# Kernel tuning notes

Measured on AMD Instinct MI355X. Metric: run time of the kernel, lower is better.

Reference implementation:

```python
import jax, jax.numpy as jnp
import numpy as np

H = 128  # hidden size

def _lstm_layer(x, Wih, Whh, bih, bhh):
    # x: [B, T, D]; Wih: [4H, D]; Whh: [4H, H]; biases: [4H]
    B, T, _ = x.shape
    # Precompute input contribution for all timesteps (one big GEMM)
    xg = jnp.einsum('btd,gd->btg', x, Wih) + bih + bhh  # [B, T, 4H]
    xg = jnp.swapaxes(xg, 0, 1)  # time-major [T, B, 4H]

    def step(carry, xt):
        h, c = carry
        gates = xt + h @ Whh.T  # [B, 4H]
        i, f, g, o = jnp.split(gates, 4, axis=-1)
        i = jax.nn.sigmoid(i)
        f = jax.nn.sigmoid(f)
        g = jnp.tanh(g)
        o = jax.nn.sigmoid(o)
        c = f * c + i * g
        h = o * jnp.tanh(c)
        return (h, c), h

    h0 = jnp.zeros((B, H), dtype=x.dtype)
    c0 = jnp.zeros((B, H), dtype=x.dtype)
    (_, _), hs = jax.lax.scan(step, (h0, c0), xg)
    return jnp.swapaxes(hs, 0, 1)  # [B, T, H]


def setup_inputs() -> dict:
    key = jax.random.key(0)
    ks = jax.random.split(key, 9)
    B, T, D = 32, 2048, 64
    s0 = 1.0 / np.sqrt(H)
    x = jax.random.normal(ks[0], (B, T, D), dtype=jnp.float32)
    # layer 0: input dim 64, layer 1: input dim 128 (torch gate order i,f,g,o)
    Wih0 = jax.random.uniform(ks[1], (4 * H, D), jnp.float32, -s0, s0)
    Whh0 = jax.random.uniform(ks[2], (4 * H, H), jnp.float32, -s0, s0)
    bih0 = jax.random.uniform(ks[3], (4 * H,), jnp.float32, -s0, s0)
    bhh0 = jax.random.uniform(ks[4], (4 * H,), jnp.float32, -s0, s0)
    Wih1 = jax.random.uniform(ks[5], (4 * H, H), jnp.float32, -s0, s0)
    Whh1 = jax.random.uniform(ks[6], (4 * H, H), jnp.float32, -s0, s0)
    bih1 = jax.random.uniform(ks[7], (4 * H,), jnp.float32, -s0, s0)
    bhh1 = jax.random.uniform(ks[8], (4 * H,), jnp.float32, -s0, s0)
    return {"x": x, "Wih0": Wih0, "Whh0": Whh0, "bih0": bih0, "bhh0": bhh0,
            "Wih1": Wih1, "Whh1": Whh1, "bih1": bih1, "bhh1": bhh1}


def reference(x, Wih0, Whh0, bih0, bhh0, Wih1, Whh1, bih1, bhh1):
    h = _lstm_layer(x, Wih0, Whh0, bih0, bhh0)
    h = _lstm_layer(h, Wih1, Whh1, bih1, bhh1)
    return h  # [B, T, H] full hidden-state sequence of the top layer
```

## Files before the change

kernel.cpp:

```cpp
#include <hip/hip_runtime.h>

#define TLEN 2048
#define BATCH 32
#define DIN 64
#define HID 128
#define RING 256
#define CHK 8
#define WRS 68

typedef _Float16 f16;
typedef _Float16 h2 __attribute__((ext_vector_type(2)));
typedef float f4 __attribute__((ext_vector_type(4)));
typedef unsigned int u32;

#if defined(__has_builtin)
#if __has_builtin(__builtin_amdgcn_fdot2)
#define FDOT2(a, b, c) __builtin_amdgcn_fdot2((a), (b), (c), false)
#endif
#endif
#ifndef FDOT2
#define FDOT2(a, b, c) ((c) + (float)(a).x * (float)(b).x + (float)(a).y * (float)(b).y)
#endif
#define DOT2U(wu, hv, acc) FDOT2(__builtin_bit_cast(h2, (wu)), (hv), (acc))

#if defined(__has_builtin)
#if __has_builtin(__builtin_amdgcn_exp2f)
#define FEXP2(x) __builtin_amdgcn_exp2f(x)
#endif
#if __has_builtin(__builtin_amdgcn_rcpf)
#define FRCP(x) __builtin_amdgcn_rcpf(x)
#endif
#endif
#ifndef FEXP2
#define FEXP2(x) __expf((x) * 0.69314718f)
#endif
#ifndef FRCP
#define FRCP(x) (1.0f / (x))
#endif

__device__ __forceinline__ float sigm(float x) {
    return FRCP(1.0f + FEXP2(-1.44269504f * x));
}
__device__ __forceinline__ float tanh_c(float x) {
    x = fminf(fmaxf(x, -15.0f), 15.0f);
    float e = FEXP2(2.88539008f * x);
    return (e - 1.0f) * FRCP(e + 1.0f);
}
__device__ __forceinline__ void qreduce(float (&v)[4]) {
    #pragma unroll
    for (int m = 0; m < 4; ++m) {
        v[m] += __shfl_xor(v[m], 1, 4);
        v[m] += __shfl_xor(v[m], 2, 4);
    }
}

__device__ __forceinline__ u32 aload_rlx(const u32* p) {
    return __hip_atomic_load(p, __ATOMIC_RELAXED, __HIP_MEMORY_SCOPE_AGENT);
}
__device__ __forceinline__ u32 aload_acq(const u32* p) {
    return __hip_atomic_load(p, __ATOMIC_ACQUIRE, __HIP_MEMORY_SCOPE_AGENT);
}
__device__ __forceinline__ void astore_rlx(u32* p, u32 v) {
    __hip_atomic_store(p, v, __ATOMIC_RELAXED, __HIP_MEMORY_SCOPE_AGENT);
}
__device__ __forceinline__ void astore_rel(u32* p, u32 v) {
    __hip_atomic_store(p, v, __ATOMIC_RELEASE, __HIP_MEMORY_SCOPE_AGENT);
}

__device__ __forceinline__ void stage_weights(const float* __restrict__ W,
                                              u32* __restrict__ wl, int t0) {
    const float2* src2 = (const float2*)W;
    for (int idx = t0; idx < 512 * 64; idx += 512) {
        const int row = idx >> 6, d = idx & 63;
        float2 v = src2[(size_t)row * 64 + d];
        h2 x; x.x = (f16)v.x; x.y = (f16)v.y;
        wl[(size_t)row * WRS + d] = __builtin_bit_cast(u32, x);
    }
}

__device__ __forceinline__ void dot_wlds(const u32* __restrict__ wl,
                                         int rg, int kg,
                                         const u32* __restrict__ hsl,
                                         float (&p)[4]) {
    uint4 hq[4];
    #pragma unroll
    for (int i4 = 0; i4 < 4; ++i4) hq[i4] = *(const uint4*)&hsl[i4 * 4];
    #pragma unroll
    for (int m = 0; m < 4; ++m) {
        const u32* wb = wl + (size_t)(rg + 128 * m) * WRS + kg * 16;
        #pragma unroll
        for (int i4 = 0; i4 < 4; ++i4) {
            const uint4 wq = *(const uint4*)&wb[i4 * 4];
            const u32* hw = (const u32*)&hq[i4];
            p[m] = DOT2U(wq.x, __builtin_bit_cast(h2, hw[0]), p[m]);
            p[m] = DOT2U(wq.y, __builtin_bit_cast(h2, hw[1]), p[m]);
            p[m] = DOT2U(wq.z, __builtin_bit_cast(h2, hw[2]), p[m]);
            p[m] = DOT2U(wq.w, __builtin_bit_cast(h2, hw[3]), p[m]);
        }
    }
}

__global__ __launch_bounds__(512) void xg_precompute(
    const float* __restrict__ X, const float* __restrict__ Wih0,
    const float* __restrict__ bih0, const float* __restrict__ bhh0,
    f16* __restrict__ XG)
{
    __shared__ float xs[16][DIN];
    const int blk = blockIdx.x;
    const int b   = blk / (TLEN / 16);
    const int tc  = blk % (TLEN / 16);
    const int j   = threadIdx.x;
    const int row = (j >> 2) + 128 * (j & 3);

    const float* xsrc = X + ((size_t)b * TLEN + (size_t)tc * 16) * DIN;
    for (int i = j; i < 16 * DIN; i += 512) ((float*)xs)[i] = xsrc[i];
    __syncthreads();

    f4 w[16];
    const f4* wp = (const f4*)(Wih0 + (size_t)row * DIN);
    #pragma unroll
    for (int i = 0; i < 16; ++i) w[i] = wp[i];
    const float bias = bih0[row] + bhh0[row];

    f16* dst = XG + ((size_t)b * TLEN + (size_t)tc * 16) * 512 + j;
    #pragma unroll 4
    for (int t = 0; t < 16; ++t) {
        float acc = bias;
        const f4* xv = (const f4*)&xs[t][0];
        #pragma unroll
        for (int i = 0; i < 16; ++i) {
            f4 x4 = xv[i];
            acc += w[i][0] * x4[0] + w[i][1] * x4[1] + w[i][2] * x4[2] + w[i][3] * x4[3];
        }
        dst[(size_t)t * 512] = (f16)acc;
    }
}

__global__ __launch_bounds__(512) void lstm2_pipe(
    const f16* __restrict__ XG0,
    const float* __restrict__ Whh0,
    const float* __restrict__ Wih1, const float* __restrict__ Whh1,
    const float* __restrict__ bih1, const float* __restrict__ bhh1,
    float* __restrict__ Out,
    u32* __restrict__ H0g,
    u32* __restrict__ XG1,
    u32* __restrict__ Flags)
{
    __shared__ alignas(16) u32 pool[39040];

    const int role = blockIdx.x / BATCH;
    const int b    = blockIdx.x % BATCH;
    const int t0   = threadIdx.x;
    const int rg   = t0 >> 2;
    const int kg   = t0 & 3;

    u32* F0 = Flags + (size_t)b * 16;
    u32* F1 = Flags + (size_t)(32 + b) * 16;
    u32* C2 = Flags + (size_t)(64 + b) * 16;

    if (role == 0) {
        stage_weights(Whh0, pool, t0);
        u32* hl = pool + 34816;
        if (t0 < 128) hl[t0] = 0u;
        float c0 = 0.0f;
        const f16* xgp = XG0 + (size_t)b * TLEN * 512 + t0;
        u32* h0out = H0g + (size_t)b * TLEN * 64;
        f16 xga = xgp[0];
        f16 xgb = xgp[512];
        __syncthreads();

        for (int t = 0; t < TLEN; ++t) {
            const int cur = t & 1, prv = cur ^ 1;
            const float xgv = (float)xga;
            xga = xgb;
            { int tn = (t + 2 < TLEN) ? t + 2 : TLEN - 1; xgb = xgp[(size_t)tn * 512]; }

            float p[4];
            #pragma unroll
            for (int m = 0; m < 4; ++m) p[m] = (kg == m) ? xgv : 0.0f;
            dot_wlds(pool, rg, kg, hl + prv * 64 + kg * 16, p);
            qreduce(p);
            float ii = sigm(p[0]), ff = sigm(p[1]);
            float gg = tanh_c(p[2]), oo = sigm(p[3]);
            c0 = ff * c0 + ii * gg;
            if (kg == 0) {
                h2 hv2; hv2.x = (f16)(oo * tanh_c(c0)); hv2.y = hv2.x;
                f16* hf = (f16*)(hl + cur * 64);
                hf[rg] = hv2.x;
            }
            __syncthreads();
            if (t0 < 64)
                astore_rlx(&h0out[(size_t)t * 64 + t0], hl[cur * 64 + t0]);
            if (t0 == 0 && (t & (CHK - 1)) == (CHK - 1))
                astore_rel(F0, (u32)(t + 1));
        }
    } else if (role == 1) {
        stage_weights(Wih1, pool, t0);
        u32* h0c = pool + 34816;
        const int rowk = rg + 128 * kg;
        const float B1 = bih1[rowk] + bhh1[rowk];
        u32* H0in = H0g + (size_t)b * TLEN * 64;
        u32* xout = XG1 + (size_t)b * RING * 512;
        u32 sc = 0;
        __syncthreads();

        for (int c = 0; c < TLEN / CHK; ++c) {
            const int tbase = c * CHK;
            if (t0 == 0) {
                u32 av; long g = 0;
                do { av = aload_acq(F0);
                     if (av >= (u32)(tbase + CHK)) break;
                     __builtin_amdgcn_s_sleep(2);
                } while (++g < 50000000L);
                if (tbase + CHK > (int)sc + (RING - 64)) {
                    g = 0;
                    do { sc = aload_rlx(C2);
                         if (tbase + CHK <= (int)sc + (RING - 64)) break;
                         __builtin_amdgcn_s_sleep(2);
                    } while (++g < 50000000L);
                }
            }
            __syncthreads();
            h0c[t0] = aload_rlx(&H0in[(size_t)tbase * 64 + t0]);
            __syncthreads();

            #pragma unroll
            for (int s = 0; s < CHK; ++s) {
                const int t = tbase + s;
                float p[4];
                #pragma unroll
                for (int m = 0; m < 4; ++m) p[m] = (kg == m) ? B1 : 0.0f;
                dot_wlds(pool, rg, kg, h0c + s * 64 + kg * 16, p);
                qreduce(p);
                astore_rlx(&xout[(size_t)(t & (RING - 1)) * 512 + t0],
                           __builtin_bit_cast(u32, p[kg]));
            }
            asm volatile("s_waitcnt vmcnt(0)" ::: "memory");
            __syncthreads();
            if (t0 == 0) astore_rel(F1, (u32)(tbase + CHK));
        }
    } else {
        stage_weights(Whh1, pool, t0);
        u32* xgc = pool + 34816;
        u32* hl  = pool + 38912;
        if (t0 < 128) hl[t0] = 0u;
        u32* xin = XG1 + (size_t)b * RING * 512;
        float c1 = 0.0f;
        __syncthreads();

        for (int c = 0; c < TLEN / CHK; ++c) {
            const int tbase = c * CHK;
            if (t0 == 0) {
                u32 av; long g = 0;
                do { av = aload_acq(F1);
                     if (av >= (u32)(tbase + CHK)) break;
                     __builtin_amdgcn_s_sleep(2);
                } while (++g < 50000000L);
            }
            __syncthreads();
            const size_t rbase = (size_t)(tbase & (RING - 1)) * 512;
            #pragma unroll
            for (int k = 0; k < CHK; ++k)
                xgc[k * 512 + t0] = aload_rlx(&xin[rbase + k * 512 + t0]);
            __syncthreads();

            #pragma unroll 1
            for (int s = 0; s < CHK; ++s) {
                const int t = tbase + s;
                const int cur = t & 1, prv = cur ^ 1;
                const float xgv = __builtin_bit_cast(float, xgc[s * 512 + t0]);

                float q[4];
                #pragma unroll
                for (int m = 0; m < 4; ++m) q[m] = (kg == m) ? xgv : 0.0f;
                dot_wlds(pool, rg, kg, hl + prv * 64 + kg * 16, q);
                qreduce(q);
                float ii = sigm(q[0]), ff = sigm(q[1]);
                float gg = tanh_c(q[2]), oo = sigm(q[3]);
                c1 = ff * c1 + ii * gg;
                float h1v = oo * tanh_c(c1);
                if (kg == 0) {
                    f16* hf = (f16*)(hl + cur * 64);
                    hf[rg] = (f16)h1v;
                    Out[((size_t)b * TLEN + t) * HID + rg] = h1v;
                }
                __syncthreads();
            }
            if (t0 == 0 && (c & 3) == 3)
                astore_rlx(C2, (u32)(tbase + CHK));
        }
    }
}

__global__ __launch_bounds__(512, 2) void lstm2_persist(
    const float* __restrict__ X,
    const float* __restrict__ Wih0, const float* __restrict__ Whh0,
    const float* __restrict__ bih0, const float* __restrict__ bhh0,
    const float* __restrict__ Wih1, const float* __restrict__ Whh1,
    const float* __restrict__ bih1, const float* __restrict__ bhh1,
    float* __restrict__ Out)
{
    __shared__ unsigned int wih0_lds[512 * 33];
    __shared__ f16 h0buf[2][HID];
    __shared__ f16 h1buf[2][HID];

    const int b  = blockIdx.x;
    const int t  = threadIdx.x;
    const int rg = t >> 2;
    const int kg = t & 3;

    {
        const float2* src = (const float2*)(Wih0 + t * DIN);
        #pragma unroll
        for (int i = 0; i < 32; ++i) {
            float2 v = src[i];
            h2 p; p.x = (f16)v.x; p.y = (f16)v.y;
            wih0_lds[t * 33 + i] = __builtin_bit_cast(unsigned int, p);
        }
    }
    if (t < HID) {
        h0buf[0][t] = (f16)0.0f; h0buf[1][t] = (f16)0.0f;
        h1buf[0][t] = (f16)0.0f; h1buf[1][t] = (f16)0.0f;
    }

    h2 whh0[4][16], wih1[4][16], whh1[4][16];
    float bi0[4], bi1[4];
    #pragma unroll
    for (int m = 0; m < 4; ++m) {
        const int row = rg + 128 * m;
        const float2* a = (const float2*)(Whh0 + row * HID + kg * 32);
        const float2* c = (const float2*)(Wih1 + row * HID + kg * 32);
        const float2* d = (const float2*)(Whh1 + row * HID + kg * 32);
        #pragma unroll
        for (int i = 0; i < 16; ++i) {
            float2 v; h2 w;
            v = a[i]; w.x = (f16)v.x; w.y = (f16)v.y; whh0[m][i] = w;
            v = c[i]; w.x = (f16)v.x; w.y = (f16)v.y; wih1[m][i] = w;
            v = d[i]; w.x = (f16)v.x; w.y = (f16)v.y; whh1[m][i] = w;
        }
        bi0[m] = (kg == 0) ? (bih0[row] + bhh0[row]) : 0.0f;
        bi1[m] = (kg == 0) ? (bih1[row] + bhh1[row]) : 0.0f;
    }

    float c0 = 0.0f, c1 = 0.0f;
    __syncthreads();

    f4 xA[4], xB[4];
    {
        const f4* xp = (const f4*)(X + ((size_t)b * TLEN) * DIN + kg * 16);
        #pragma unroll
        for (int j = 0; j < 4; ++j) xA[j] = xp[j];
    }

    auto step = [&](int tt, f4 (&xc)[4], f4 (&xn)[4]) {
        const int cur = tt & 1, nxt = cur ^ 1;
        h2 xh[8];
        const float* xf = (const float*)xc;
        #pragma unroll
        for (int j = 0; j < 8; ++j) {
            h2 p; p.x = (f16)xf[2 * j]; p.y = (f16)xf[2 * j + 1];
            xh[j] = p;
        }
        {
            const int tn = (tt + 1 < TLEN) ? tt + 1 : TLEN - 1;
            const f4* xp = (const f4*)(X + ((size_t)b * TLEN + tn) * DIN + kg * 16);
            #pragma unroll
            for (int j = 0; j < 4; ++j) xn[j] = xp[j];
        }
        float p0[4];
        #pragma unroll
        for (int m = 0; m < 4; ++m) p0[m] = bi0[m];
        #pragma unroll
        for (int m = 0; m < 4; ++m) {
            const unsigned int* wr = &wih0_lds[(rg + 128 * m) * 33 + kg * 8];
            #pragma unroll
            for (int i = 0; i < 8; ++i) {
                h2 w = __builtin_bit_cast(h2, wr[i]);
                p0[m] = FDOT2(w, xh[i], p0[m]);
            }
        }
        {
            const unsigned int* hr = (const unsigned int*)&h0buf[cur][0];
            #pragma unroll
            for (int i = 0; i < 16; ++i) {
                h2 hv = __builtin_bit_cast(h2, hr[kg * 16 + i]);
                #pragma unroll
                for (int m = 0; m < 4; ++m)
                    p0[m] = FDOT2(whh0[m][i], hv, p0[m]);
            }
        }
        qreduce(p0);
        {
            float ii = sigm(p0[0]), ff = sigm(p0[1]);
            float gg = tanh_c(p0[2]), oo = sigm(p0[3]);
            c0 = ff * c0 + ii * gg;
            float h0v = oo * tanh_c(c0);
            if (kg == 0) h0buf[nxt][rg] = (f16)h0v;
        }
        __syncthreads();
        float q[4];
        #pragma unroll
        for (int m = 0; m < 4; ++m) q[m] = bi1[m];
        {
            const unsigned int* hr = (const unsigned int*)&h0buf[nxt][0];
            #pragma unroll
            for (int i = 0; i < 16; ++i) {
                h2 hv = __builtin_bit_cast(h2, hr[kg * 16 + i]);
                #pragma unroll
                for (int m = 0; m < 4; ++m)
                    q[m] = FDOT2(wih1[m][i], hv, q[m]);
            }
        }
        {
            const unsigned int* hr = (const unsigned int*)&h1buf[cur][0];
            #pragma unroll
            for (int i = 0; i < 16; ++i) {
                h2 hv = __builtin_bit_cast(h2, hr[kg * 16 + i]);
                #pragma unroll
                for (int m = 0; m < 4; ++m)
                    q[m] = FDOT2(whh1[m][i], hv, q[m]);
            }
        }
        qreduce(q);
        {
            float ii = sigm(q[0]), ff = sigm(q[1]);
            float gg = tanh_c(q[2]), oo = sigm(q[3]);
            c1 = ff * c1 + ii * gg;
            float h1v = oo * tanh_c(c1);
            if (kg == 0) {
                h1buf[nxt][rg] = (f16)h1v;
                Out[((size_t)b * TLEN + tt) * HID + rg] = h1v;
            }
        }
        __syncthreads();
    };

    for (int tt = 0; tt < TLEN; tt += 2) {
        step(tt, xA, xB);
        step(tt + 1, xB, xA);
    }
}

extern "C" void kernel_launch(void* const* d_in, const int* in_sizes, int n_in,
                              void* d_out, int out_size, void* d_ws, size_t ws_size,
                              hipStream_t stream) {
    const float* X    = (const float*)d_in[0];
    const float* Wih0 = (const float*)d_in[1];
    const float* Whh0 = (const float*)d_in[2];
    const float* bih0 = (const float*)d_in[3];
    const float* bhh0 = (const float*)d_in[4];
    const float* Wih1 = (const float*)d_in[5];
    const float* Whh1 = (const float*)d_in[6];
    const float* bih1 = (const float*)d_in[7];
    const float* bhh1 = (const float*)d_in[8];
    float* Out = (float*)d_out;

    const size_t XG0_B  = (size_t)BATCH * TLEN * 512 * 2;
    const size_t H0_B   = (size_t)BATCH * TLEN * 64 * 4;
    const size_t XG1_B  = (size_t)BATCH * RING * 512 * 4;
    const size_t FLAG_B = 96 * 16 * 4;
    const size_t NEED   = XG0_B + H0_B + XG1_B + FLAG_B;

    if (ws_size >= NEED) {
        char* ws = (char*)d_ws;
        f16* XG0   = (f16*)ws;
        u32* H0g   = (u32*)(ws + XG0_B);
        u32* XG1   = (u32*)(ws + XG0_B + H0_B);
        u32* Flags = (u32*)(ws + XG0_B + H0_B + XG1_B);

        hipMemsetAsync(Flags, 0, FLAG_B, stream);
        xg_precompute<<<dim3(BATCH * (TLEN / 16)), dim3(512), 0, stream>>>(
            X, Wih0, bih0, bhh0, XG0);
        lstm2_pipe<<<dim3(3 * BATCH), dim3(512), 0, stream>>>(
            XG0, Whh0, Wih1, Whh1, bih1, bhh1, Out, H0g, XG1, Flags);
    } else {
        lstm2_persist<<<dim3(BATCH), dim3(512), 0, stream>>>(
            X, Wih0, Whh0, bih0, bhh0, Wih1, Whh1, bih1, bhh1, Out);
    }
}
```

Before: 2.160 ms.

## Split recurrent weights between LDS and per-step global loads

Only the first two gate blocks (i,f) of each weight matrix are staged in LDS. The g,o halves are prepacked into a coalesced fp16 global layout by a new kernel and reloaded from global/L2 at every timestep, where an asm barrier stops them being hoisted into registers. LDS use per block drops from about 156KB to about 86KB, which cuts the LDS read traffic per step and may allow better occupancy or co-residency. The cost is 128 bytes per thread of global loads on the latency-critical recurrent path each step.

```diff
diff --git a/kernel.cpp b/kernel.cpp
--- a/kernel.cpp
+++ b/kernel.cpp
@@ -67,10 +67,10 @@
     __hip_atomic_store(p, v, __ATOMIC_RELEASE, __HIP_MEMORY_SCOPE_AGENT);
 }
 
-__device__ __forceinline__ void stage_weights(const float* __restrict__ W,
-                                              u32* __restrict__ wl, int t0) {
+__device__ __forceinline__ void stage_w2(const float* __restrict__ W,
+                                         u32* __restrict__ wl, int t0) {
     const float2* src2 = (const float2*)W;
-    for (int idx = t0; idx < 512 * 64; idx += 512) {
+    for (int idx = t0; idx < 256 * 64; idx += 512) {
         const int row = idx >> 6, d = idx & 63;
         float2 v = src2[(size_t)row * 64 + d];
         h2 x; x.x = (f16)v.x; x.y = (f16)v.y;
@@ -78,25 +78,64 @@
     }
 }
 
-__device__ __forceinline__ void dot_wlds(const u32* __restrict__ wl,
+__device__ __forceinline__ void dot_step(const u32* __restrict__ wl,
                                          int rg, int kg,
                                          const u32* __restrict__ hsl,
-                                         float (&p)[4]) {
+                                         uintptr_t wga, float (&p)[4]) {
+    uint4 wq[8];
+    const uint4* wgp = (const uint4*)wga;
+    #pragma unroll
+    for (int qq = 0; qq < 8; ++qq) wq[qq] = wgp[(size_t)qq * 512];
+
     uint4 hq[4];
     #pragma unroll
     for (int i4 = 0; i4 < 4; ++i4) hq[i4] = *(const uint4*)&hsl[i4 * 4];
-    #pragma unroll
-    for (int m = 0; m < 4; ++m) {
+
+    #pragma unroll
+    for (int m = 0; m < 2; ++m) {
         const u32* wb = wl + (size_t)(rg + 128 * m) * WRS + kg * 16;
         #pragma unroll
         for (int i4 = 0; i4 < 4; ++i4) {
-            const uint4 wq = *(const uint4*)&wb[i4 * 4];
+            const uint4 wv = *(const uint4*)&wb[i4 * 4];
             const u32* hw = (const u32*)&hq[i4];
-            p[m] = DOT2U(wq.x, __builtin_bit_cast(h2, hw[0]), p[m]);
-            p[m] = DOT2U(wq.y, __builtin_bit_cast(h2, hw[1]), p[m]);
-            p[m] = DOT2U(wq.z, __builtin_bit_cast(h2, hw[2]), p[m]);
-            p[m] = DOT2U(wq.w, __builtin_bit_cast(h2, hw[3]), p[m]);
-        }
+            p[m] = DOT2U(wv.x, __builtin_bit_cast(h2, hw[0]), p[m]);
+            p[m] = DOT2U(wv.y, __builtin_bit_cast(h2, hw[1]), p[m]);
+            p[m] = DOT2U(wv.z, __builtin_bit_cast(h2, hw[2]), p[m]);
+            p[m] = DOT2U(wv.w, __builtin_bit_cast(h2, hw[3]), p[m]);
+        }
+    }
+    #pragma unroll
+    for (int mh = 0; mh < 2; ++mh) {
+        #pragma unroll
+        for (int i4 = 0; i4 < 4; ++i4) {
+            const uint4 wv = wq[mh * 4 + i4];
+            const u32* hw = (const u32*)&hq[i4];
+            p[2 + mh] = DOT2U(wv.x, __builtin_bit_cast(h2, hw[0]), p[2 + mh]);
+            p[2 + mh] = DOT2U(wv.y, __builtin_bit_cast(h2, hw[1]), p[2 + mh]);
+            p[2 + mh] = DOT2U(wv.z, __builtin_bit_cast(h2, hw[2]), p[2 + mh]);
+            p[2 + mh] = DOT2U(wv.w, __builtin_bit_cast(h2, hw[3]), p[2 + mh]);
+        }
+    }
+}
+
+__global__ __launch_bounds__(512) void w_prepack(
+    const float* __restrict__ W0, const float* __restrict__ W1,
+    const float* __restrict__ W2, u32* __restrict__ WG)
+{
+    const float* W = (blockIdx.x == 0) ? W0 : (blockIdx.x == 1) ? W1 : W2;
+    u32* dst = WG + (size_t)blockIdx.x * 16384;
+    const int t0 = threadIdx.x, rg = t0 >> 2, kg = t0 & 3;
+    #pragma unroll
+    for (int qq = 0; qq < 8; ++qq) {
+        const int m = 2 + (qq >> 2), j = qq & 3;
+        const float* s = W + (size_t)(rg + 128 * m) * HID + kg * 32 + j * 8;
+        u32 out[4];
+        #pragma unroll
+        for (int d = 0; d < 4; ++d) {
+            h2 x; x.x = (f16)s[2 * d]; x.y = (f16)s[2 * d + 1];
+            out[d] = __builtin_bit_cast(u32, x);
+        }
+        *(uint4*)&dst[((size_t)qq * 512 + t0) * 4] = *(const uint4*)out;
     }
 }
 
@@ -144,9 +183,10 @@
     float* __restrict__ Out,
     u32* __restrict__ H0g,
     u32* __restrict__ XG1,
-    u32* __restrict__ Flags)
+    u32* __restrict__ Flags,
+    const u32* __restrict__ WG)
 {
-    __shared__ alignas(16) u32 pool[39040];
+    __shared__ alignas(16) u32 pool[21632];
 
     const int role = blockIdx.x / BATCH;
     const int b    = blockIdx.x % BATCH;
@@ -158,9 +198,11 @@
     u32* F1 = Flags + (size_t)(32 + b) * 16;
     u32* C2 = Flags + (size_t)(64 + b) * 16;
 
+    uintptr_t wga = (uintptr_t)(WG + (size_t)role * 16384 + (size_t)t0 * 4);
+
     if (role == 0) {
-        stage_weights(Whh0, pool, t0);
-        u32* hl = pool + 34816;
+        stage_w2(Whh0, pool, t0);
+        u32* hl = pool + 17408;
         if (t0 < 128) hl[t0] = 0u;
         float c0 = 0.0f;
         const f16* xgp = XG0 + (size_t)b * TLEN * 512 + t0;
@@ -175,18 +217,18 @@
             xga = xgb;
             { int tn = (t + 2 < TLEN) ? t + 2 : TLEN - 1; xgb = xgp[(size_t)tn * 512]; }
 
+            asm volatile("" : "+v"(wga));
             float p[4];
             #pragma unroll
             for (int m = 0; m < 4; ++m) p[m] = (kg == m) ? xgv : 0.0f;
-            dot_wlds(pool, rg, kg, hl + prv * 64 + kg * 16, p);
+            dot_step(pool, rg, kg, hl + prv * 64 + kg * 16, wga, p);
             qreduce(p);
             float ii = sigm(p[0]), ff = sigm(p[1]);
             float gg = tanh_c(p[2]), oo = sigm(p[3]);
             c0 = ff * c0 + ii * gg;
             if (kg == 0) {
-                h2 hv2; hv2.x = (f16)(oo * tanh_c(c0)); hv2.y = hv2.x;
                 f16* hf = (f16*)(hl + cur * 64);
-                hf[rg] = hv2.x;
+                hf[rg] = (f16)(oo * tanh_c(c0));
             }
             __syncthreads();
             if (t0 < 64)
@@ -195,8 +237,8 @@
                 astore_rel(F0, (u32)(t + 1));
         }
     } else if (role == 1) {
-        stage_weights(Wih1, pool, t0);
-        u32* h0c = pool + 34816;
+        stage_w2(Wih1, pool, t0);
+        u32* h0c = pool + 17408;
         const int rowk = rg + 128 * kg;
         const float B1 = bih1[rowk] + bhh1[rowk];
         u32* H0in = H0g + (size_t)b * TLEN * 64;
@@ -227,10 +269,11 @@
             #pragma unroll
             for (int s = 0; s < CHK; ++s) {
                 const int t = tbase + s;
+                asm volatile("" : "+v"(wga));
                 float p[4];
                 #pragma unroll
                 for (int m = 0; m < 4; ++m) p[m] = (kg == m) ? B1 : 0.0f;
-                dot_wlds(pool, rg, kg, h0c + s * 64 + kg * 16, p);
+                dot_step(pool, rg, kg, h0c + s * 64 + kg * 16, wga, p);
                 qreduce(p);
                 astore_rlx(&xout[(size_t)(t & (RING - 1)) * 512 + t0],
                            __builtin_bit_cast(u32, p[kg]));
@@ -240,9 +283,9 @@
             if (t0 == 0) astore_rel(F1, (u32)(tbase + CHK));
         }
     } else {
-        stage_weights(Whh1, pool, t0);
-        u32* xgc = pool + 34816;
-        u32* hl  = pool + 38912;
+        stage_w2(Whh1, pool, t0);
+        u32* xgc = pool + 17408;
+        u32* hl  = pool + 21504;
         if (t0 < 128) hl[t0] = 0u;
         u32* xin = XG1 + (size_t)b * RING * 512;
         float c1 = 0.0f;
@@ -270,10 +313,11 @@
                 const int cur = t & 1, prv = cur ^ 1;
                 const float xgv = __builtin_bit_cast(float, xgc[s * 512 + t0]);
 
+                asm volatile("" : "+v"(wga));
                 float q[4];
                 #pragma unroll
                 for (int m = 0; m < 4; ++m) q[m] = (kg == m) ? xgv : 0.0f;
-                dot_wlds(pool, rg, kg, hl + prv * 64 + kg * 16, q);
+                dot_step(pool, rg, kg, hl + prv * 64 + kg * 16, wga, q);
                 qreduce(q);
                 float ii = sigm(q[0]), ff = sigm(q[1]);
                 float gg = tanh_c(q[2]), oo = sigm(q[3]);
@@ -458,21 +502,24 @@
     const size_t XG0_B  = (size_t)BATCH * TLEN * 512 * 2;
     const size_t H0_B   = (size_t)BATCH * TLEN * 64 * 4;
     const size_t XG1_B  = (size_t)BATCH * RING * 512 * 4;
+    const size_t WG_B   = (size_t)3 * 16384 * 4;
     const size_t FLAG_B = 96 * 16 * 4;
-    const size_t NEED   = XG0_B + H0_B + XG1_B + FLAG_B;
+    const size_t NEED   = XG0_B + H0_B + XG1_B + WG_B + FLAG_B;
 
     if (ws_size >= NEED) {
         char* ws = (char*)d_ws;
         f16* XG0   = (f16*)ws;
         u32* H0g   = (u32*)(ws + XG0_B);
         u32* XG1   = (u32*)(ws + XG0_B + H0_B);
-        u32* Flags = (u32*)(ws + XG0_B + H0_B + XG1_B);
+        u32* WG    = (u32*)(ws + XG0_B + H0_B + XG1_B);
+        u32* Flags = (u32*)(ws + XG0_B + H0_B + XG1_B + WG_B);
 
         hipMemsetAsync(Flags, 0, FLAG_B, stream);
+        w_prepack<<<dim3(3), dim3(512), 0, stream>>>(Whh0, Wih1, Whh1, WG);
         xg_precompute<<<dim3(BATCH * (TLEN / 16)), dim3(512), 0, stream>>>(
             X, Wih0, bih0, bhh0, XG0);
         lstm2_pipe<<<dim3(3 * BATCH), dim3(512), 0, stream>>>(
-            XG0, Whh0, Wih1, Whh1, bih1, bhh1, Out, H0g, XG1, Flags);
+            XG0, Whh0, Wih1, Whh1, bih1, bhh1, Out, H0g, XG1, Flags, WG);
     } else {
         lstm2_persist<<<dim3(BATCH), dim3(512), 0, stream>>>(
             X, Wih0, Whh0, bih0, bhh0, Wih1, Whh1, bih1, bhh1, Out);
```

New measurement: 2.895 ms. +34.0%, slower.
